# Optimization experiments

Measured on AMD Instinct MI355X. Metric: run time of the kernel, lower is better.

The kernel has to match this reference:

```python
import jax, jax.numpy as jnp
import numpy as np

IN, HID, OUT = 8, 64, 2

def setup_inputs() -> dict:
    key = jax.random.key(0)
    ks = jax.random.split(key, 8)
    s_ih = 1.0 / np.sqrt(HID)
    x = jax.random.normal(ks[0], (8192, 512, IN), dtype=jnp.float32)
    W_ih = jax.random.uniform(ks[1], (4 * HID, IN), minval=-s_ih, maxval=s_ih, dtype=jnp.float32)
    W_hh = jax.random.uniform(ks[2], (4 * HID, HID), minval=-s_ih, maxval=s_ih, dtype=jnp.float32)
    b_ih = jax.random.uniform(ks[3], (4 * HID,), minval=-s_ih, maxval=s_ih, dtype=jnp.float32)
    b_hh = jax.random.uniform(ks[4], (4 * HID,), minval=-s_ih, maxval=s_ih, dtype=jnp.float32)
    s_fc = 1.0 / np.sqrt(HID)
    W_fc = jax.random.uniform(ks[5], (OUT, HID), minval=-s_fc, maxval=s_fc, dtype=jnp.float32)
    b_fc = jax.random.uniform(ks[6], (OUT,), minval=-s_fc, maxval=s_fc, dtype=jnp.float32)
    return {"x": x, "W_ih": W_ih, "W_hh": W_hh, "b_ih": b_ih, "b_hh": b_hh, "W_fc": W_fc, "b_fc": b_fc}

def reference(x, W_ih, W_hh, b_ih, b_hh, W_fc, b_fc):
    B = x.shape[0]
    # Precompute input projections for all timesteps: [T, B, 4H]
    xg = jnp.einsum('bti,gi->tbg', x, W_ih) + b_ih + b_hh

    def step(carry, xg_t):
        h, c = carry
        gates = xg_t + h @ W_hh.T  # [B, 4H]
        i, f, g, o = jnp.split(gates, 4, axis=-1)  # torch gate order i,f,g,o
        i = jax.nn.sigmoid(i); f = jax.nn.sigmoid(f)
        g = jnp.tanh(g); o = jax.nn.sigmoid(o)
        c = f * c + i * g
        h = o * jnp.tanh(c)
        return (h, c), None

    h0 = jnp.zeros((B, HID), dtype=x.dtype)
    c0 = jnp.zeros((B, HID), dtype=x.dtype)
    (h_last, _), _ = jax.lax.scan(step, (h0, c0), xg)
    return h_last @ W_fc.T + b_fc  # [B, 2]
```

## Files before the change

### kernel.cpp

```cpp
#include <hip/hip_runtime.h>

#define T 512
#define HID 64
#define BLK_B 16
#define TS 64
#define NCHUNK (T / TS)

typedef __attribute__((ext_vector_type(8))) _Float16 f16x8;
typedef __attribute__((ext_vector_type(4))) _Float16 f16x4;
typedef __attribute__((ext_vector_type(4))) float f32x4;

__device__ __forceinline__ float fast_rcp(float x) { return __builtin_amdgcn_rcpf(x); }
__device__ __forceinline__ float sig_f(float x) { return fast_rcp(1.0f + __expf(-x)); }
__device__ __forceinline__ float th_f(float x)  { return 1.0f - 2.0f * fast_rcp(__expf(2.0f * x) + 1.0f); }

#define MFMA(a, b, c) __builtin_amdgcn_mfma_f32_16x16x32_f16((a), (b), (c), 0, 0, 0)

__global__ __launch_bounds__(256, 2) void lstm_mfma_kernel(
    const float* __restrict__ x,
    const float* __restrict__ W_ih,
    const float* __restrict__ W_hh,
    const float* __restrict__ b_ih,
    const float* __restrict__ b_hh,
    const float* __restrict__ W_fc,
    const float* __restrict__ b_fc,
    float* __restrict__ out)
{
    __shared__ alignas(16) _Float16 arena[28672];
    _Float16* xb    = arena;
    _Float16* hbase = arena + TS * BLK_B * 8;

    const int tid  = threadIdx.x;
    const int w    = tid >> 6;
    const int lane = tid & 63;
    const int colb = lane & 15;
    const int grp  = lane >> 4;
    const int batch0 = blockIdx.x * BLK_B;

#define DECL_Q(q) f16x8 whi##q##_0, whi##q##_1, wih##q; f32x4 bias##q;
    DECL_Q(0) DECL_Q(1) DECL_Q(2) DECL_Q(3)
#undef DECL_Q

    f16x8 zz;
    #pragma unroll
    for (int e = 0; e < 8; ++e) zz[e] = (_Float16)0.0f;

#define LOAD_Q(q) {                                                        \
        int gate = 64 * q + 16 * w + colb;                                 \
        const float* wr = W_hh + gate * 64 + grp * 8;                      \
        _Pragma("unroll")                                                  \
        for (int e = 0; e < 8; ++e) {                                      \
            whi##q##_0[e] = (_Float16)wr[e];                               \
            whi##q##_1[e] = (_Float16)wr[32 + e];                          \
        }                                                                  \
        const float* wi = W_ih + gate * 8;                                 \
        f16x8 ih;                                                          \
        _Pragma("unroll")                                                  \
        for (int e = 0; e < 8; ++e) ih[e] = (_Float16)wi[e];               \
        wih##q = (grp == 0) ? ih : zz;    \
        int gb = 64 * q + 16 * w + grp * 4;                                \
        bias##q.x = b_ih[gb + 0] + b_hh[gb + 0];                           \
        bias##q.y = b_ih[gb + 1] + b_hh[gb + 1];                           \
        bias##q.z = b_ih[gb + 2] + b_hh[gb + 2];                           \
        bias##q.w = b_ih[gb + 3] + b_hh[gb + 3];                           \
    }
    LOAD_Q(0) LOAD_Q(1) LOAD_Q(2) LOAD_Q(3)
#undef LOAD_Q

    #pragma unroll
    for (int i = 0; i < 9; ++i) hbase[tid * 9 + i] = (_Float16)0.0f;

    f32x4 cst = {0.0f, 0.0f, 0.0f, 0.0f};

    int cur = 0;
    #pragma unroll 1
    for (int tc = 0; tc < NCHUNK; ++tc) {
        {
            int sb = tid >> 4, st = tid & 15;
            #pragma unroll
            for (int r = 0; r < 4; ++r) {
                int t = st + r * 16;
                const float* xg = x + ((size_t)(batch0 + sb) * T + (size_t)tc * TS + t) * 8;
                f16x8 v;
                #pragma unroll
                for (int e = 0; e < 8; ++e) v[e] = (_Float16)xg[e];
                *(f16x8*)(xb + (t * BLK_B + sb) * 8) = v;
            }
        }
        __syncthreads();

        #pragma unroll 1
        for (int tt = 0; tt < TS; ++tt) {
            const _Float16* hc = hbase + cur * 1152;
            f16x8 bh0 = *(const f16x8*)(hc + colb * 72 + grp * 8);
            f16x8 bh1 = *(const f16x8*)(hc + colb * 72 + 32 + grp * 8);
            f16x8 bx  = *(const f16x8*)(xb + (tt * BLK_B + colb) * 8);

#define QMM(q, acc)                                           \
            f32x4 acc = MFMA(wih##q, bx, bias##q);            \
            acc = MFMA(whi##q##_0, bh0, acc);                 \
            acc = MFMA(whi##q##_1, bh1, acc);
            QMM(0, a0) QMM(1, a1) QMM(2, a2) QMM(3, a3)
#undef QMM

            f32x4 gi, gf, gg, go;
            gi.x = sig_f(a0.x); gi.y = sig_f(a0.y); gi.z = sig_f(a0.z); gi.w = sig_f(a0.w);
            gf.x = sig_f(a1.x); gf.y = sig_f(a1.y); gf.z = sig_f(a1.z); gf.w = sig_f(a1.w);
            gg.x = th_f(a2.x);  gg.y = th_f(a2.y);  gg.z = th_f(a2.z);  gg.w = th_f(a2.w);
            go.x = sig_f(a3.x); go.y = sig_f(a3.y); go.z = sig_f(a3.z); go.w = sig_f(a3.w);

            cst.x = fmaf(gf.x, cst.x, gi.x * gg.x);
            cst.y = fmaf(gf.y, cst.y, gi.y * gg.y);
            cst.z = fmaf(gf.z, cst.z, gi.z * gg.z);
            cst.w = fmaf(gf.w, cst.w, gi.w * gg.w);
            float h0 = go.x * th_f(cst.x);
            float h1 = go.y * th_f(cst.y);
            float h2 = go.z * th_f(cst.z);
            float h3 = go.w * th_f(cst.w);

            {
                _Float16* hw = hbase + (cur ^ 1) * 1152 + colb * 72 + 16 * w + grp * 4;
                f16x4 hv;
                hv[0] = (_Float16)h0; hv[1] = (_Float16)h1;
                hv[2] = (_Float16)h2; hv[3] = (_Float16)h3;
                *(f16x4*)hw = hv;
            }

            __syncthreads();
            cur ^= 1;
        }
    }

    {
        const _Float16* ph = hbase + cur * 1152 + (tid >> 4) * 72 + (tid & 15) * 4;
        int b = tid >> 4, q4 = (tid & 15) * 4;
        float h0 = (float)ph[0];
        float h1 = (float)ph[1];
        float h2 = (float)ph[2];
        float h3 = (float)ph[3];
        float s0 = h0 * W_fc[q4] + h1 * W_fc[q4 + 1] + h2 * W_fc[q4 + 2] + h3 * W_fc[q4 + 3];
        float s1 = h0 * W_fc[64 + q4] + h1 * W_fc[64 + q4 + 1] + h2 * W_fc[64 + q4 + 2] + h3 * W_fc[64 + q4 + 3];
        #pragma unroll
        for (int off = 1; off < 16; off <<= 1) {
            s0 += __shfl_xor(s0, off, 64);
            s1 += __shfl_xor(s1, off, 64);
        }
        if ((tid & 15) == 0) {
            out[(size_t)(batch0 + b) * 2 + 0] = s0 + b_fc[0];
            out[(size_t)(batch0 + b) * 2 + 1] = s1 + b_fc[1];
        }
    }
}

extern "C" void kernel_launch(void* const* d_in, const int* in_sizes, int n_in,
                              void* d_out, int out_size, void* d_ws, size_t ws_size,
                              hipStream_t stream) {
    const float* x    = (const float*)d_in[0];
    const float* W_ih = (const float*)d_in[1];
    const float* W_hh = (const float*)d_in[2];
    const float* b_ih = (const float*)d_in[3];
    const float* b_hh = (const float*)d_in[4];
    const float* W_fc = (const float*)d_in[5];
    const float* b_fc = (const float*)d_in[6];
    float* out = (float*)d_out;

    dim3 grid(8192 / BLK_B);
    dim3 block(256);
    lstm_mfma_kernel<<<grid, block, 0, stream>>>(x, W_ih, W_hh, b_ih, b_hh,
                                                 W_fc, b_fc, out);
}
```

Baseline: 368.3 us.

## Split waves into MFMA and activation roles ping-ponging two batch halves

Each block now holds 32 batch rows split into two halves, with 512 threads. Four waves compute the gate MFMAs for one half while the other four apply the activations and the cell update for the other half. Gate pre-activations pass between them through swizzled fp32 LDS. The aim is to overlap the tensor-core matmul with the transcendental-heavy elementwise work inside the serial recurrence. Activations now use exp2 intrinsics and packed fp16 conversion. The cost is a barrier at every half-step, extra LDS traffic for the gates, and fewer blocks in the grid.

```diff
diff --git a/kernel.cpp b/kernel.cpp
--- a/kernel.cpp
+++ b/kernel.cpp
@@ -1,22 +1,27 @@
 #include <hip/hip_runtime.h>
+#include <cmath>
 
 #define T 512
 #define HID 64
-#define BLK_B 16
-#define TS 64
-#define NCHUNK (T / TS)
+#define BLK_B 32
+#define TS 32
+#define LOG2E 1.44269504f
 
 typedef __attribute__((ext_vector_type(8))) _Float16 f16x8;
-typedef __attribute__((ext_vector_type(4))) _Float16 f16x4;
 typedef __attribute__((ext_vector_type(4))) float f32x4;
 
 __device__ __forceinline__ float fast_rcp(float x) { return __builtin_amdgcn_rcpf(x); }
-__device__ __forceinline__ float sig_f(float x) { return fast_rcp(1.0f + __expf(-x)); }
-__device__ __forceinline__ float th_f(float x)  { return 1.0f - 2.0f * fast_rcp(__expf(2.0f * x) + 1.0f); }
+__device__ __forceinline__ float fast_exp2(float x) { return __builtin_amdgcn_exp2f(x); }
+__device__ __forceinline__ float sig_f(float x) {
+    return fast_rcp(1.0f + fast_exp2(-LOG2E * x));
+}
+__device__ __forceinline__ float th_f(float x) {
+    return 1.0f - 2.0f * fast_rcp(1.0f + fast_exp2((2.0f * LOG2E) * x));
+}
 
 #define MFMA(a, b, c) __builtin_amdgcn_mfma_f32_16x16x32_f16((a), (b), (c), 0, 0, 0)
 
-__global__ __launch_bounds__(256, 2) void lstm_mfma_kernel(
+__global__ __launch_bounds__(512) void lstm_rs_kernel(
     const float* __restrict__ x,
     const float* __restrict__ W_ih,
     const float* __restrict__ W_hh,
@@ -26,21 +31,23 @@
     const float* __restrict__ b_fc,
     float* __restrict__ out)
 {
-    __shared__ alignas(16) _Float16 arena[28672];
-    _Float16* xb    = arena;
-    _Float16* hbase = arena + TS * BLK_B * 8;
+    __shared__ alignas(16) float arena[16128];
+    float*     gbase = arena;
+    _Float16*  xb    = (_Float16*)(arena + 8192);
+    _Float16*  hbase = xb + 8192;
 
     const int tid  = threadIdx.x;
-    const int w    = tid >> 6;
+    const int wv   = tid >> 6;
     const int lane = tid & 63;
     const int colb = lane & 15;
     const int grp  = lane >> 4;
     const int batch0 = blockIdx.x * BLK_B;
+    const bool isM = (wv < 4);
+    const int w = isM ? wv : (wv - 4);
 
 #define DECL_Q(q) f16x8 whi##q##_0, whi##q##_1, wih##q; f32x4 bias##q;
     DECL_Q(0) DECL_Q(1) DECL_Q(2) DECL_Q(3)
 #undef DECL_Q
-
     f16x8 zz;
     #pragma unroll
     for (int e = 0; e < 8; ++e) zz[e] = (_Float16)0.0f;
@@ -57,7 +64,7 @@
         f16x8 ih;                                                          \
         _Pragma("unroll")                                                  \
         for (int e = 0; e < 8; ++e) ih[e] = (_Float16)wi[e];               \
-        wih##q = (grp == 0) ? ih : zz;    \
+        wih##q = (grp == 0) ? ih : zz;                                     \
         int gb = 64 * q + 16 * w + grp * 4;                                \
         bias##q.x = b_ih[gb + 0] + b_hh[gb + 0];                           \
         bias##q.y = b_ih[gb + 1] + b_hh[gb + 1];                           \
@@ -67,73 +74,100 @@
     LOAD_Q(0) LOAD_Q(1) LOAD_Q(2) LOAD_Q(3)
 #undef LOAD_Q
 
-    #pragma unroll
-    for (int i = 0; i < 9; ++i) hbase[tid * 9 + i] = (_Float16)0.0f;
-
-    f32x4 cst = {0.0f, 0.0f, 0.0f, 0.0f};
-
-    int cur = 0;
+    for (int i = tid; i < 2304; i += 512) hbase[i] = (_Float16)0.0f;
+
+    f32x4 c0v = {0, 0, 0, 0};
+    f32x4 c1v = {0, 0, 0, 0};
+
+#define STG(gh, q, acc) {                                                  \
+        int i16 = (((colb * 4 + (q)) * 16) + 4 * w + grp) ^ colb;          \
+        *(f32x4*)((gh) + i16 * 4) = acc;                                   \
+    }
+#define MPH(half, tmod) {                                                  \
+        const _Float16* hb = hbase + (half) * 1152 + colb * 72 + grp * 8;  \
+        f16x8 bh0 = *(const f16x8*)(hb);                                   \
+        f16x8 bh1 = *(const f16x8*)(hb + 32);                              \
+        f16x8 bx  = *(const f16x8*)(xb + (tmod) * 256 + (half) * 128 + colb * 8); \
+        f32x4 a0 = MFMA(wih0, bx, bias0);                                  \
+        a0 = MFMA(whi0_0, bh0, a0);  a0 = MFMA(whi0_1, bh1, a0);           \
+        f32x4 a1 = MFMA(wih1, bx, bias1);                                  \
+        a1 = MFMA(whi1_0, bh0, a1);  a1 = MFMA(whi1_1, bh1, a1);           \
+        f32x4 a2 = MFMA(wih2, bx, bias2);                                  \
+        a2 = MFMA(whi2_0, bh0, a2);  a2 = MFMA(whi2_1, bh1, a2);           \
+        f32x4 a3 = MFMA(wih3, bx, bias3);                                  \
+        a3 = MFMA(whi3_0, bh0, a3);  a3 = MFMA(whi3_1, bh1, a3);           \
+        float* gh = gbase + (half) * 4096;                                 \
+        STG(gh, 0, a0) STG(gh, 1, a1) STG(gh, 2, a2) STG(gh, 3, a3)        \
+    }
+
+#define APH(half, CV) {                                                    \
+        const float* gh = gbase + (half) * 4096;                           \
+        int i0 = (((colb * 4 + 0) * 16) + 4 * w + grp) ^ colb;             \
+        int i1 = (((colb * 4 + 1) * 16) + 4 * w + grp) ^ colb;             \
+        int i2 = (((colb * 4 + 2) * 16) + 4 * w + grp) ^ colb;             \
+        int i3 = (((colb * 4 + 3) * 16) + 4 * w + grp) ^ colb;             \
+        f32x4 ai = *(const f32x4*)(gh + i0 * 4);                           \
+        f32x4 af = *(const f32x4*)(gh + i1 * 4);                           \
+        f32x4 ag = *(const f32x4*)(gh + i2 * 4);                           \
+        f32x4 ao = *(const f32x4*)(gh + i3 * 4);                           \
+        float gi0 = sig_f(ai.x), gi1 = sig_f(ai.y), gi2 = sig_f(ai.z), gi3 = sig_f(ai.w); \
+        float gf0 = sig_f(af.x), gf1 = sig_f(af.y), gf2 = sig_f(af.z), gf3 = sig_f(af.w); \
+        float gg0 = th_f(ag.x),  gg1 = th_f(ag.y),  gg2 = th_f(ag.z),  gg3 = th_f(ag.w);  \
+        float go0 = sig_f(ao.x), go1 = sig_f(ao.y), go2 = sig_f(ao.z), go3 = sig_f(ao.w); \
+        CV.x = fmaf(gf0, CV.x, gi0 * gg0);                                 \
+        CV.y = fmaf(gf1, CV.y, gi1 * gg1);                                 \
+        CV.z = fmaf(gf2, CV.z, gi2 * gg2);                                 \
+        CV.w = fmaf(gf3, CV.w, gi3 * gg3);                                 \
+        float h0 = go0 * th_f(CV.x);                                       \
+        float h1 = go1 * th_f(CV.y);                                       \
+        float h2 = go2 * th_f(CV.z);                                       \
+        float h3 = go3 * th_f(CV.w);                                       \
+        auto p01 = __builtin_amdgcn_cvt_pkrtz(h0, h1);                     \
+        auto p23 = __builtin_amdgcn_cvt_pkrtz(h2, h3);                     \
+        uint2 st;                                                          \
+        st.x = __builtin_bit_cast(unsigned int, p01);                      \
+        st.y = __builtin_bit_cast(unsigned int, p23);                      \
+        *(uint2*)(hbase + (half) * 1152 + colb * 72 + 16 * w + grp * 4) = st; \
+    }
+
+#define STAGE(tstart) {                                                    \
+        int sb = tid >> 4, st_ = tid & 15;                                 \
+        _Pragma("unroll")                                                  \
+        for (int r = 0; r < 2; ++r) {                                      \
+            int tt = st_ + r * 16;                                         \
+            const float* xg = x + ((size_t)(batch0 + sb) * T + (tstart) + tt) * 8; \
+            f16x8 v;                                                       \
+            _Pragma("unroll")                                              \
+            for (int e = 0; e < 8; ++e) v[e] = (_Float16)xg[e];            \
+            *(f16x8*)(xb + (tt * 32 + sb) * 8) = v;                        \
+        }                                                                  \
+    }
+
+    STAGE(0)
+    __syncthreads();
+
+    if (isM) { MPH(0, 0) }
+    __syncthreads();
+
     #pragma unroll 1
-    for (int tc = 0; tc < NCHUNK; ++tc) {
-        {
-            int sb = tid >> 4, st = tid & 15;
-            #pragma unroll
-            for (int r = 0; r < 4; ++r) {
-                int t = st + r * 16;
-                const float* xg = x + ((size_t)(batch0 + sb) * T + (size_t)tc * TS + t) * 8;
-                f16x8 v;
-                #pragma unroll
-                for (int e = 0; e < 8; ++e) v[e] = (_Float16)xg[e];
-                *(f16x8*)(xb + (t * BLK_B + sb) * 8) = v;
-            }
+    for (int t = 0; t < T; ++t) {
+        const int tmod = t & (TS - 1);
+        if (isM) { MPH(1, tmod) } else { APH(0, c0v) }
+        __syncthreads();
+        if (t == T - 1) break;
+        if (((t + 1) & (TS - 1)) == 0) {
+            STAGE(t + 1)
+            __syncthreads();
         }
+        if (isM) { MPH(0, (t + 1) & (TS - 1)) } else { APH(1, c1v) }
         __syncthreads();
-
-        #pragma unroll 1
-        for (int tt = 0; tt < TS; ++tt) {
-            const _Float16* hc = hbase + cur * 1152;
-            f16x8 bh0 = *(const f16x8*)(hc + colb * 72 + grp * 8);
-            f16x8 bh1 = *(const f16x8*)(hc + colb * 72 + 32 + grp * 8);
-            f16x8 bx  = *(const f16x8*)(xb + (tt * BLK_B + colb) * 8);
-
-#define QMM(q, acc)                                           \
-            f32x4 acc = MFMA(wih##q, bx, bias##q);            \
-            acc = MFMA(whi##q##_0, bh0, acc);                 \
-            acc = MFMA(whi##q##_1, bh1, acc);
-            QMM(0, a0) QMM(1, a1) QMM(2, a2) QMM(3, a3)
-#undef QMM
-
-            f32x4 gi, gf, gg, go;
-            gi.x = sig_f(a0.x); gi.y = sig_f(a0.y); gi.z = sig_f(a0.z); gi.w = sig_f(a0.w);
-            gf.x = sig_f(a1.x); gf.y = sig_f(a1.y); gf.z = sig_f(a1.z); gf.w = sig_f(a1.w);
-            gg.x = th_f(a2.x);  gg.y = th_f(a2.y);  gg.z = th_f(a2.z);  gg.w = th_f(a2.w);
-            go.x = sig_f(a3.x); go.y = sig_f(a3.y); go.z = sig_f(a3.z); go.w = sig_f(a3.w);
-
-            cst.x = fmaf(gf.x, cst.x, gi.x * gg.x);
-            cst.y = fmaf(gf.y, cst.y, gi.y * gg.y);
-            cst.z = fmaf(gf.z, cst.z, gi.z * gg.z);
-            cst.w = fmaf(gf.w, cst.w, gi.w * gg.w);
-            float h0 = go.x * th_f(cst.x);
-            float h1 = go.y * th_f(cst.y);
-            float h2 = go.z * th_f(cst.z);
-            float h3 = go.w * th_f(cst.w);
-
-            {
-                _Float16* hw = hbase + (cur ^ 1) * 1152 + colb * 72 + 16 * w + grp * 4;
-                f16x4 hv;
-                hv[0] = (_Float16)h0; hv[1] = (_Float16)h1;
-                hv[2] = (_Float16)h2; hv[3] = (_Float16)h3;
-                *(f16x4*)hw = hv;
-            }
-
-            __syncthreads();
-            cur ^= 1;
-        }
-    }
+    }
+    if (!isM) { APH(1, c1v) }
+    __syncthreads();
 
     {
-        const _Float16* ph = hbase + cur * 1152 + (tid >> 4) * 72 + (tid & 15) * 4;
         int b = tid >> 4, q4 = (tid & 15) * 4;
+        const _Float16* ph = hbase + (b >> 4) * 1152 + (b & 15) * 72 + q4;
         float h0 = (float)ph[0];
         float h1 = (float)ph[1];
         float h2 = (float)ph[2];
@@ -150,6 +184,10 @@
             out[(size_t)(batch0 + b) * 2 + 1] = s1 + b_fc[1];
         }
     }
+#undef MPH
+#undef APH
+#undef STG
+#undef STAGE
 }
 
 extern "C" void kernel_launch(void* const* d_in, const int* in_sizes, int n_in,
@@ -165,7 +203,7 @@
     float* out = (float*)d_out;
 
     dim3 grid(8192 / BLK_B);
-    dim3 block(256);
-    lstm_mfma_kernel<<<grid, block, 0, stream>>>(x, W_ih, W_hh, b_ih, b_hh,
-                                                 W_fc, b_fc, out);
-}
+    dim3 block(512);
+    lstm_rs_kernel<<<grid, block, 0, stream>>>(x, W_ih, W_hh, b_ih, b_hh,
+                                               W_fc, b_fc, out);
+}
```

New measurement: 452.2 us. +22.8%, slower.
